# Performance work log

Hardware: AMD Instinct MI355X
Metric: run time of the kernel (lower is better)

Reference implementation:

```python
import jax, jax.numpy as jnp
import numpy as np

EMBED_DIM = 1024
NUM_HEADS = 16
HEAD_DIM = EMBED_DIM // NUM_HEADS
B, S = 2, 2048
NEG = -1e20


def setup_inputs() -> dict:
    key = jax.random.key(0)
    ks = jax.random.split(key, 8)
    scale = 0.02
    return {
        "query": jax.random.normal(ks[0], (B, S, EMBED_DIM), jnp.float32),
        "keys": jax.random.normal(ks[1], (B, S, EMBED_DIM), jnp.float32),
        "values": jax.random.normal(ks[2], (B, S, EMBED_DIM), jnp.float32),
        "mask": jax.random.randint(ks[3], (1, 1, S, S), 0, 2, jnp.int32),
        "Wq": jax.random.normal(ks[4], (EMBED_DIM, EMBED_DIM), jnp.float32) * scale,
        "Wk": jax.random.normal(ks[5], (EMBED_DIM, EMBED_DIM), jnp.float32) * scale,
        "Wv": jax.random.normal(ks[6], (EMBED_DIM, EMBED_DIM), jnp.float32) * scale,
        "Wo": jax.random.normal(ks[7], (EMBED_DIM, EMBED_DIM), jnp.float32) * scale,
        "bo": jnp.zeros((EMBED_DIM,), jnp.float32),
    }


def reference(query, keys, values, mask, Wq, Wk, Wv, Wo, bo):
    N, Lq, _ = query.shape
    Lk = keys.shape[1]
    # torch nn.Linear: y = x @ W.T  (bias=False for Q/K/V)
    Q = (query @ Wq.T).reshape(N, Lq, NUM_HEADS, HEAD_DIM)
    K = (keys @ Wk.T).reshape(N, Lk, NUM_HEADS, HEAD_DIM)
    V = (values @ Wv.T).reshape(N, Lk, NUM_HEADS, HEAD_DIM)
    # NOTE: source scales by sqrt(embed_dim), not sqrt(head_dim) — kept faithful.
    energy = jnp.einsum("nqhd,nkhd->nhqk", Q, K) / jnp.sqrt(
        jnp.asarray(EMBED_DIM, Q.dtype)
    )
    energy = jnp.where(mask == 0, jnp.asarray(NEG, energy.dtype), energy)
    attention = jax.nn.softmax(energy, axis=3)
    out = jnp.einsum("nhqk,nkhd->nqhd", attention, V).reshape(N, Lq, EMBED_DIM)
    return out @ Wo.T + bo
```

## Files before the change

### kernel.cpp

```cpp
#include <hip/hip_runtime.h>
#include <stdint.h>

typedef __bf16 bf16;
typedef __bf16 bf16x4 __attribute__((ext_vector_type(4)));
typedef __bf16 bf16x8 __attribute__((ext_vector_type(8)));
typedef float f32x4 __attribute__((ext_vector_type(4)));
typedef float f32x16 __attribute__((ext_vector_type(16)));
typedef unsigned int uintx2 __attribute__((ext_vector_type(2)));
typedef unsigned int uintx4 __attribute__((ext_vector_type(4)));

#define MFMA16(a, b, c) __builtin_amdgcn_mfma_f32_16x16x32_bf16((a), (b), (c), 0, 0, 0)
#define MFMA32(a, b, c) __builtin_amdgcn_mfma_f32_32x32x16_bf16((a), (b), (c), 0, 0, 0)

__device__ __forceinline__ void gload16(const bf16* g, bf16* l) {
    __builtin_amdgcn_global_load_lds(
        (const __attribute__((address_space(1))) void*)g,
        (__attribute__((address_space(3))) void*)l, 16, 0, 0);
}

__device__ __forceinline__ float fast_exp2(float x) {
#if __has_builtin(__builtin_amdgcn_exp2f)
    return __builtin_amdgcn_exp2f(x);
#else
    return exp2f(x);
#endif
}

__global__ __launch_bounds__(256) void cvt_kernel(
    const float* __restrict__ q, const float* __restrict__ k, const float* __restrict__ v,
    const float* __restrict__ wq, const float* __restrict__ wk,
    const float* __restrict__ wv, const float* __restrict__ wo,
    const int* __restrict__ mask,
    bf16* __restrict__ qb, bf16* __restrict__ kb, bf16* __restrict__ vb,
    bf16* __restrict__ wqb, bf16* __restrict__ wkb, bf16* __restrict__ wvb,
    bf16* __restrict__ wob, unsigned long long* __restrict__ maskb)
{
    int z = blockIdx.z;
    if (z == 7) {
        int t16 = blockIdx.x * 256 + threadIdx.x;
        if (t16 >= 262144) return;
        const int4* mp = (const int4*)mask + (size_t)t16 * 4;
        unsigned bits = 0;
#pragma unroll
        for (int c = 0; c < 4; ++c) {
            int4 a = mp[c];
            bits |= (unsigned)(a.x != 0) << (c * 4 + 0);
            bits |= (unsigned)(a.y != 0) << (c * 4 + 1);
            bits |= (unsigned)(a.z != 0) << (c * 4 + 2);
            bits |= (unsigned)(a.w != 0) << (c * 4 + 3);
        }
        unsigned long long u = (unsigned long long)bits << (16 * (threadIdx.x & 3));
        u |= __shfl_xor(u, 1, 64);
        u |= __shfl_xor(u, 2, 64);
        if ((threadIdx.x & 3) == 0) maskb[t16 >> 2] = u;
        return;
    }
    const float* src; bf16* dst; int n;
    switch (z) {
        case 0:  src = q;  dst = qb;  n = 4194304; break;
        case 1:  src = k;  dst = kb;  n = 4194304; break;
        case 2:  src = v;  dst = vb;  n = 4194304; break;
        case 3:  src = wq; dst = wqb; n = 1048576; break;
        case 4:  src = wk; dst = wkb; n = 1048576; break;
        case 5:  src = wv; dst = wvb; n = 1048576; break;
        default: src = wo; dst = wob; n = 1048576; break;
    }
    int i = (blockIdx.x * 256 + threadIdx.x) * 8;
    if (i >= n) return;
    float4 f0 = *(const float4*)(src + i);
    float4 f1 = *(const float4*)(src + i + 4);
    bf16x8 o;
    o[0] = (bf16)f0.x; o[1] = (bf16)f0.y; o[2] = (bf16)f0.z; o[3] = (bf16)f0.w;
    o[4] = (bf16)f1.x; o[5] = (bf16)f1.y; o[6] = (bf16)f1.z; o[7] = (bf16)f1.w;
    *(bf16x8*)(dst + i) = o;
}

__global__ __launch_bounds__(256) void gemm_qkv_kernel(
    const bf16* __restrict__ A0, const bf16* __restrict__ A1, const bf16* __restrict__ A2,
    const bf16* __restrict__ B0, const bf16* __restrict__ B1, const bf16* __restrict__ B2,
    bf16* __restrict__ C0, bf16* __restrict__ C1, bf16* __restrict__ Vt)
{
    constexpr int BUFSZ = 8192;
    __shared__ bf16 smem[3 * BUFSZ];

    const int f = blockIdx.x + 8 * blockIdx.y + 256 * blockIdx.z;
    const int xcd = f & 7, sidx = f >> 3;
    const int z  = sidx >> 5;
    const int m0 = (xcd * 4 + (sidx & 3)) * 128;
    const int n0 = ((sidx >> 2) & 7) * 128;

    const bf16* A = (z == 0) ? A0 : (z == 1) ? A1 : A2;
    const bf16* B = (z == 0) ? B0 : (z == 1) ? B1 : B2;

    const int tid  = threadIdx.x;
    const int lane = tid & 63;
    const int wave = tid >> 6;
    const int quad = lane >> 4;
    const int l16  = lane & 15;
    const int wm = (wave >> 1) * 64;
    const int wn = (wave & 1) * 64;

    const int lrow = lane >> 2;
    const int lcol = (lane & 3) * 8;

    f32x4 acc[4][4] = {};

    const bf16* Ag = A + (size_t)(m0 + lrow) * 1024 + lcol;
    const bf16* Bg = B + (size_t)(n0 + lrow) * 1024 + lcol;

    bf16* buf0 = smem;
    bf16* buf1 = smem + BUFSZ;
    bf16* buf2 = smem + 2 * BUFSZ;

    auto stage = [&](bf16* base, int k0) {
#pragma unroll
        for (int j = 0; j < 2; ++j)
            gload16(Ag + (size_t)(wave * 32 + j * 16) * 1024 + k0,
                    base + (wave * 32 + j * 16) * 32);
        bf16* Btb = base + 4096;
#pragma unroll
        for (int j = 0; j < 2; ++j)
            gload16(Bg + (size_t)(wave * 32 + j * 16) * 1024 + k0,
                    Btb + (wave * 32 + j * 16) * 32);
    };

    auto step = [&](bf16* cb, bf16* sb, int k0) {
        if (k0 == 992) {
            asm volatile("s_waitcnt vmcnt(0)" ::: "memory");
        } else {
            asm volatile("s_waitcnt vmcnt(4)" ::: "memory");
        }
        __builtin_amdgcn_s_barrier();
        __builtin_amdgcn_sched_barrier(0);
        if (k0 + 64 < 1024) stage(sb, k0 + 64);

        const bf16* Btb = cb + 4096;
        bf16x8 af[4], bg[4];
#pragma unroll
        for (int i = 0; i < 4; ++i)
            af[i] = *(const bf16x8*)(cb + (wm + i * 16 + l16) * 32 + quad * 8);
#pragma unroll
        for (int j = 0; j < 4; ++j)
            bg[j] = *(const bf16x8*)(Btb + (wn + j * 16 + l16) * 32 + quad * 8);
#pragma unroll
        for (int i = 0; i < 4; ++i)
#pragma unroll
            for (int j = 0; j < 4; ++j)
                acc[i][j] = MFMA16(af[i], bg[j], acc[i][j]);
    };

    stage(buf0, 0);
    stage(buf1, 32);
    for (int k0 = 0; k0 < 960; k0 += 96) {
        step(buf0, buf2, k0);
        step(buf1, buf0, k0 + 32);
        step(buf2, buf1, k0 + 64);
    }
    step(buf0, buf2, 960);
    step(buf1, buf0, 992);

    if (z == 2) {
        __syncthreads();
        const int qsw = ((quad & 1) << 1) | (quad >> 1);
#pragma unroll
        for (int i = 0; i < 4; ++i)
#pragma unroll
            for (int j = 0; j < 4; ++j) {
                int e  = wn + j * 16 + l16;
                int sp = wm + i * 16 + qsw * 4;
                bf16x4 v4;
#pragma unroll
                for (int r = 0; r < 4; ++r) v4[r] = (bf16)acc[i][j][r];
                *(bf16x4*)(smem + e * 136 + sp) = v4;
            }
        __syncthreads();
        const int bq = m0 >> 11;
        const int srow = m0 & 2047;
#pragma unroll
        for (int c = 0; c < 2; ++c) {
            int idx = c * 256 + tid;
            int e = idx >> 2, sc = (idx & 3) * 32;
            bf16* dst = Vt + (size_t)(bq * 1024 + n0 + e) * 2048 + srow + sc;
#pragma unroll
            for (int kk = 0; kk < 4; ++kk)
                *(bf16x8*)(dst + kk * 8) =
                    *(const bf16x8*)(smem + e * 136 + sc + kk * 8);
        }
        return;
    }
    bf16* C = (z == 0) ? C0 : C1;
    const float cs = (z == 0) ? 0.0450842200277800f : 1.0f;
#pragma unroll
    for (int i = 0; i < 4; ++i)
#pragma unroll
        for (int j = 0; j < 4; ++j) {
            int row = m0 + wm + i * 16 + quad * 4;
            int col = n0 + wn + j * 16 + l16;
#pragma unroll
            for (int r = 0; r < 4; ++r)
                C[(row + r) * 1024 + col] = (bf16)(acc[i][j][r] * cs);
        }
}

__global__ __launch_bounds__(512) void gemm_out_kernel(
    const bf16* __restrict__ Ab, const bf16* __restrict__ Bb,
    const float* __restrict__ bias, float* __restrict__ outf)
{
    constexpr int BUFSZ = 4096 + 2048;
    __shared__ bf16 smem[2 * 3 * BUFSZ];

    const int f = blockIdx.x + 8 * blockIdx.y;
    const int xcd = f & 7, sidx = f >> 3;
    const int m0 = (xcd * 4 + (sidx & 3)) * 128;
    const int n0 = (sidx >> 2) * 64;

    const int tid  = threadIdx.x;
    const int lane = tid & 63;
    const int wave = tid >> 6;
    const int half = wave >> 2;
    const int w4   = wave & 3;
    const int quad = lane >> 4;
    const int l16  = lane & 15;
    const int wm = (w4 >> 1) * 64;
    const int wn = (w4 & 1) * 32;

    const int lrow = lane >> 2;
    const int lcol = (lane & 3) * 8;
    const int kbase = half * 512;

    f32x4 acc[4][2] = {};

    const bf16* Ag = Ab + (size_t)(m0 + lrow) * 1024 + lcol + kbase;
    const bf16* Bg = Bb + (size_t)(n0 + lrow) * 1024 + lcol + kbase;

    bf16* hb   = smem + half * 3 * BUFSZ;
    bf16* buf0 = hb;
    bf16* buf1 = hb + BUFSZ;
    bf16* buf2 = hb + 2 * BUFSZ;

    auto stage = [&](bf16* base, int k0) {
#pragma unroll
        for (int j = 0; j < 2; ++j)
            gload16(Ag + (size_t)(w4 * 32 + j * 16) * 1024 + k0,
                    base + (w4 * 32 + j * 16) * 32);
        gload16(Bg + (size_t)(w4 * 16) * 1024 + k0, base + 4096 + (w4 * 16) * 32);
    };

    auto step = [&](bf16* cb, bf16* sb, int k0) {
        if (k0 == 480) {
            asm volatile("s_waitcnt vmcnt(0)" ::: "memory");
        } else {
            asm volatile("s_waitcnt vmcnt(3)" ::: "memory");
        }
        __builtin_amdgcn_s_barrier();
        __builtin_amdgcn_sched_barrier(0);
        if (k0 + 64 < 512) stage(sb, k0 + 64);

        const bf16* Btb = cb + 4096;
        bf16x8 af[4], bg[2];
#pragma unroll
        for (int i = 0; i < 4; ++i)
            af[i] = *(const bf16x8*)(cb + (wm + i * 16 + l16) * 32 + quad * 8);
#pragma unroll
        for (int j = 0; j < 2; ++j)
            bg[j] = *(const bf16x8*)(Btb + (wn + j * 16 + l16) * 32 + quad * 8);
#pragma unroll
        for (int i = 0; i < 4; ++i)
#pragma unroll
            for (int j = 0; j < 2; ++j)
                acc[i][j] = MFMA16(af[i], bg[j], acc[i][j]);
    };

    stage(buf0, 0);
    stage(buf1, 32);
    for (int k0 = 0; k0 < 480; k0 += 96) {
        step(buf0, buf2, k0);
        step(buf1, buf0, k0 + 32);
        step(buf2, buf1, k0 + 64);
    }
    step(buf0, buf1, 480);

    __syncthreads();
    float* ex = (float*)smem + (w4 * 64 + lane) * 4;
    if (half == 1) {
#pragma unroll
        for (int i = 0; i < 4; ++i) {
            *(f32x4*)(ex + (i + 0) * 1024) = acc[i][0];
            *(f32x4*)(ex + (i + 4) * 1024) = acc[i][1];
        }
    }
    __syncthreads();
    if (half == 0) {
#pragma unroll
        for (int i = 0; i < 4; ++i) {
            f32x4 t0 = *(const f32x4*)(ex + (i + 0) * 1024);
            f32x4 t1 = *(const f32x4*)(ex + (i + 4) * 1024);
#pragma unroll
            for (int j = 0; j < 4; ++j) {
                acc[i][0][j] += t0[j];
                acc[i][1][j] += t1[j];
            }
        }
#pragma unroll
        for (int j = 0; j < 2; ++j) {
            int col = n0 + wn + j * 16 + l16;
            float bj = bias[col];
#pragma unroll
            for (int i = 0; i < 4; ++i) {
                int row = m0 + wm + i * 16 + quad * 4;
#pragma unroll
                for (int r = 0; r < 4; ++r)
                    outf[(row + r) * 1024 + col] = acc[i][j][r] + bj;
            }
        }
    }
}

__global__ __launch_bounds__(512, 4) void flash_kernel(
    const bf16* __restrict__ Q, const bf16* __restrict__ K, const bf16* __restrict__ Vt,
    const unsigned long long* __restrict__ maskb, bf16* __restrict__ O)
{
    __shared__ char smem[65536];

    const int tid  = threadIdx.x;
    const int lane = tid & 63;
    const int wave = tid >> 6;
    const int half = wave >> 2;
    const int w4   = wave & 3;
    const int l32  = lane & 31;
    const int hl   = lane >> 5;
    const int l7   = lane & 7;

    const int flat = blockIdx.x + 16 * (blockIdx.y + 16 * blockIdx.z);
    const int xcd  = flat & 7;
    const int slot = flat >> 3;
    const int bh   = xcd * 4 + (slot >> 4);
    const int h  = bh & 15;
    const int b  = bh >> 4;
    const int q0 = (slot & 15) * 128;
    const int qt = q0 + w4 * 32;

    bf16* hbase = (bf16*)smem + half * 16384;
    bf16* K0 = hbase;
    bf16* K1 = hbase + 4096;
    bf16* V0 = hbase + 8192;
    bf16* V1 = hbase + 12288;

    const bf16* Qb = Q + (size_t)(b * 2048 + qt + l32) * 1024 + h * 64 + hl * 8;
    bf16x8 qf[4];
#pragma unroll
    for (int ks = 0; ks < 4; ++ks) qf[ks] = *(const bf16x8*)(Qb + ks * 16);

    bf16x8 ones;
#pragma unroll
    for (int j = 0; j < 8; ++j) ones[j] = (bf16)1.0f;

    f32x16 acc[2] = {};
    f32x16 lacc = {};

    const int dmarow = lane >> 3;
    const int dmacol = (l7 ^ dmarow) * 8;
    const bf16* Kg = K + (size_t)(b * 2048 + w4 * 16 + dmarow) * 1024 + h * 64 + dmacol;
    const bf16* Vg = Vt + (size_t)((b * 16 + h) * 64 + w4 * 16 + dmarow) * 2048 + dmacol;
    const unsigned long long* Mg = maskb + (size_t)(qt + l32) * 32 + half * 16;
    const int kbase = half * 1024;

    auto stage = [&](bf16* Kd, bf16* Vd, int ktAbs) {
        gload16(Kg + (size_t)ktAbs * 1024,       Kd + (w4 * 16) * 64);
        gload16(Kg + (size_t)(ktAbs + 8) * 1024, Kd + (w4 * 16 + 8) * 64);
        gload16(Vg + ktAbs,                      Vd + (w4 * 16) * 64);
        gload16(Vg + ktAbs + 8 * 2048,           Vd + (w4 * 16 + 8) * 64);
    };

    unsigned long long mw = Mg[0];
    stage(K0, V0, kbase);

    auto body = [&](const bf16* Kc, const bf16* Vc, bf16* Kn, bf16* Vn, int it) {
        __syncthreads();
        unsigned long long mw_next = 0;
        if (it + 1 < 16) {
            stage(Kn, Vn, kbase + (it + 1) * 64);
            mw_next = Mg[it + 1];
        }

        bf16x8 pa[4];
#pragma unroll
        for (int t = 0; t < 2; ++t) {
            f32x16 s = {};
            __builtin_amdgcn_s_setprio(1);
#pragma unroll
            for (int ks = 0; ks < 4; ++ks) {
                bf16x8 ka = *(const bf16x8*)(Kc + (t * 32 + l32) * 64 +
                                             (((ks * 2 + hl) ^ l7) * 8));
                s = MFMA32(ka, qf[ks], s);
            }
            __builtin_amdgcn_s_setprio(0);
            unsigned mwt = (unsigned)(mw >> (t * 32 + 4 * hl));
            unsigned W[4][2];
#pragma unroll
            for (int g = 0; g < 4; ++g) {
                bf16x4 pv;
#pragma unroll
                for (int r = 0; r < 4; ++r) {
                    float ev = fast_exp2(s[g * 4 + r]);
                    unsigned msk = (unsigned)((int)(mwt << (31 - (8 * g + r))) >> 31);
                    unsigned evu = __builtin_bit_cast(unsigned, ev) & msk;
                    pv[r] = (bf16)__builtin_bit_cast(float, evu);
                }
                uintx2 u = __builtin_bit_cast(uintx2, pv);
                W[g][0] = u[0];
                W[g][1] = u[1];
            }
#pragma unroll
            for (int kh = 0; kh < 2; ++kh) {
                uintx4 aw = { W[2 * kh][0], W[2 * kh][1],
                              W[2 * kh + 1][0], W[2 * kh + 1][1] };
                pa[t * 2 + kh] = __builtin_bit_cast(bf16x8, aw);
            }
        }

        __builtin_amdgcn_s_setprio(1);
#pragma unroll
        for (int dt = 0; dt < 2; ++dt)
#pragma unroll
            for (int ks = 0; ks < 4; ++ks) {
                bf16x8 vb = *(const bf16x8*)(Vc + (dt * 32 + l32) * 64 +
                                             (((ks * 2 + hl) ^ l7) * 8));
                acc[dt] = MFMA32(pa[ks], vb, acc[dt]);
            }
#pragma unroll
        for (int ks = 0; ks < 4; ++ks)
            lacc = MFMA32(pa[ks], ones, lacc);
        __builtin_amdgcn_s_setprio(0);

        mw = mw_next;
    };

    for (int it = 0; it < 16; it += 2) {
        body(K0, V0, K1, V1, it);
        body(K1, V1, K0, V0, it + 1);
    }

    __syncthreads();
    float* cb = (float*)smem;
    float* ex = cb + (w4 * 64 + lane) * 4;
    if (half == 1) {
#pragma unroll
        for (int i = 0; i < 4; ++i) {
            f32x4 t0, t1, t2;
#pragma unroll
            for (int j = 0; j < 4; ++j) {
                t0[j] = acc[0][i * 4 + j];
                t1[j] = acc[1][i * 4 + j];
                t2[j] = lacc[i * 4 + j];
            }
            *(f32x4*)(ex + (i + 0) * 1024) = t0;
            *(f32x4*)(ex + (i + 4) * 1024) = t1;
            *(f32x4*)(ex + (i + 8) * 1024) = t2;
        }
    }
    __syncthreads();
    if (half == 0) {
#pragma unroll
        for (int i = 0; i < 4; ++i) {
            f32x4 t0 = *(const f32x4*)(ex + (i + 0) * 1024);
            f32x4 t1 = *(const f32x4*)(ex + (i + 4) * 1024);
            f32x4 t2 = *(const f32x4*)(ex + (i + 8) * 1024);
#pragma unroll
            for (int j = 0; j < 4; ++j) {
                acc[0][i * 4 + j] += t0[j];
                acc[1][i * 4 + j] += t1[j];
                lacc[i * 4 + j]   += t2[j];
            }
        }

        const size_t obase = (size_t)(b * 2048 + qt) * 1024 + h * 64;
#pragma unroll
        for (int g = 0; g < 4; ++g)
#pragma unroll
            for (int r = 0; r < 4; ++r) {
                int qr = 4 * hl + 8 * g + r;
                float inv = 1.0f / lacc[g * 4 + r];
                O[obase + (size_t)qr * 1024 + l32]      = (bf16)(acc[0][g * 4 + r] * inv);
                O[obase + (size_t)qr * 1024 + 32 + l32] = (bf16)(acc[1][g * 4 + r] * inv);
            }
    }
}

extern "C" void kernel_launch(void* const* d_in, const int* in_sizes, int n_in,
                              void* d_out, int out_size, void* d_ws, size_t ws_size,
                              hipStream_t stream)
{
    const float* q  = (const float*)d_in[0];
    const float* k  = (const float*)d_in[1];
    const float* v  = (const float*)d_in[2];
    const int* mask = (const int*)d_in[3];
    const float* wq = (const float*)d_in[4];
    const float* wk = (const float*)d_in[5];
    const float* wv = (const float*)d_in[6];
    const float* wo = (const float*)d_in[7];
    const float* bo = (const float*)d_in[8];
    float* out = (float*)d_out;

    char* p = (char*)d_ws;
    auto alloc = [&](size_t bytes) {
        char* r = p;
        p += (bytes + 255) & ~(size_t)255;
        return r;
    };
    const size_t SB = (size_t)4096 * 1024 * 2;
    const size_t WB = (size_t)1024 * 1024 * 2;
    bf16* qb  = (bf16*)alloc(SB);
    bf16* kb  = (bf16*)alloc(SB);
    bf16* vb  = (bf16*)alloc(SB);
    bf16* wqb = (bf16*)alloc(WB);
    bf16* wkb = (bf16*)alloc(WB);
    bf16* wvb = (bf16*)alloc(WB);
    bf16* wob = (bf16*)alloc(WB);
    bf16* Qp  = (bf16*)alloc(SB);
    bf16* Kp  = (bf16*)alloc(SB);
    bf16* Vtp = (bf16*)alloc(SB);
    bf16* Ob  = (bf16*)alloc(SB);
    unsigned long long* maskb = (unsigned long long*)alloc(2048 * 32 * 8);

    cvt_kernel<<<dim3(2048, 1, 8), 256, 0, stream>>>(
        q, k, v, wq, wk, wv, wo, mask, qb, kb, vb, wqb, wkb, wvb, wob, maskb);

    gemm_qkv_kernel<<<dim3(8, 32, 3), 256, 0, stream>>>(
        qb, kb, vb, wqb, wkb, wvb, Qp, Kp, Vtp);

    flash_kernel<<<dim3(16, 16, 2), 512, 0, stream>>>(Qp, Kp, Vtp, maskb, Ob);

    gemm_out_kernel<<<dim3(8, 64), 512, 0, stream>>>(Ob, wob, bo, out);
}
```

Measured before the change: 226.5 us.

## Single-buffer V tile and cut flash kernel LDS to raise occupancy

The V tile goes from double-buffered to a single LDS buffer, shrinking shared memory from 64KB to 48KB, and launch bounds rise to 6 blocks/CU hint. V for the current step is now loaded at the start of each iteration alongside the next K tile, with explicit vmcnt waits and an extra barrier before the PV MFMAs. The goal is more resident waves to hide latency, at the cost of exposing V load latency within each iteration and adding a barrier per step. The mask word is also loaded synchronously each iteration instead of prefetched.

```diff
diff --git a/kernel.cpp b/kernel.cpp
--- a/kernel.cpp
+++ b/kernel.cpp
@@ -316,11 +316,11 @@
     }
 }
 
-__global__ __launch_bounds__(512, 4) void flash_kernel(
+__global__ __launch_bounds__(512, 6) void flash_kernel(
     const bf16* __restrict__ Q, const bf16* __restrict__ K, const bf16* __restrict__ Vt,
     const unsigned long long* __restrict__ maskb, bf16* __restrict__ O)
 {
-    __shared__ char smem[65536];
+    __shared__ char smem[49152];
 
     const int tid  = threadIdx.x;
     const int lane = tid & 63;
@@ -340,11 +340,10 @@
     const int q0 = (slot & 15) * 128;
     const int qt = q0 + w4 * 32;
 
-    bf16* hbase = (bf16*)smem + half * 16384;
+    bf16* hbase = (bf16*)smem + half * 12288;
     bf16* K0 = hbase;
     bf16* K1 = hbase + 4096;
-    bf16* V0 = hbase + 8192;
-    bf16* V1 = hbase + 12288;
+    bf16* Vb = hbase + 8192;
 
     const bf16* Qb = Q + (size_t)(b * 2048 + qt + l32) * 1024 + h * 64 + hl * 8;
     bf16x8 qf[4];
@@ -365,23 +364,26 @@
     const unsigned long long* Mg = maskb + (size_t)(qt + l32) * 32 + half * 16;
     const int kbase = half * 1024;
 
-    auto stage = [&](bf16* Kd, bf16* Vd, int ktAbs) {
+    auto stageK = [&](bf16* Kd, int ktAbs) {
         gload16(Kg + (size_t)ktAbs * 1024,       Kd + (w4 * 16) * 64);
         gload16(Kg + (size_t)(ktAbs + 8) * 1024, Kd + (w4 * 16 + 8) * 64);
-        gload16(Vg + ktAbs,                      Vd + (w4 * 16) * 64);
-        gload16(Vg + ktAbs + 8 * 2048,           Vd + (w4 * 16 + 8) * 64);
-    };
-
-    unsigned long long mw = Mg[0];
-    stage(K0, V0, kbase);
-
-    auto body = [&](const bf16* Kc, const bf16* Vc, bf16* Kn, bf16* Vn, int it) {
-        __syncthreads();
-        unsigned long long mw_next = 0;
-        if (it + 1 < 16) {
-            stage(Kn, Vn, kbase + (it + 1) * 64);
-            mw_next = Mg[it + 1];
-        }
+    };
+    auto stageV = [&](int ktAbs) {
+        gload16(Vg + ktAbs,            Vb + (w4 * 16) * 64);
+        gload16(Vg + ktAbs + 8 * 2048, Vb + (w4 * 16 + 8) * 64);
+    };
+
+    stageK(K0, kbase);
+
+    auto body = [&](const bf16* Kc, bf16* Kn, int it) {
+        asm volatile("s_waitcnt vmcnt(0)" ::: "memory");
+        __builtin_amdgcn_s_barrier();
+        __builtin_amdgcn_sched_barrier(0);
+        unsigned long long mw = Mg[it];
+        __builtin_amdgcn_sched_barrier(0);
+        stageV(kbase + it * 64);
+        if (it + 1 < 16) stageK(Kn, kbase + (it + 1) * 64);
+        __builtin_amdgcn_sched_barrier(0);
 
         bf16x8 pa[4];
 #pragma unroll
@@ -395,6 +397,10 @@
                 s = MFMA32(ka, qf[ks], s);
             }
             __builtin_amdgcn_s_setprio(0);
+            if (t == 0) {
+                if (it == 15) asm volatile("s_waitcnt vmcnt(2)" ::: "memory");
+                else          asm volatile("s_waitcnt vmcnt(4)" ::: "memory");
+            }
             unsigned mwt = (unsigned)(mw >> (t * 32 + 4 * hl));
             unsigned W[4][2];
 #pragma unroll
@@ -419,12 +425,17 @@
             }
         }
 
+        if (it == 15) asm volatile("s_waitcnt vmcnt(0)" ::: "memory");
+        else          asm volatile("s_waitcnt vmcnt(2)" ::: "memory");
+        __builtin_amdgcn_s_barrier();
+        __builtin_amdgcn_sched_barrier(0);
+
         __builtin_amdgcn_s_setprio(1);
 #pragma unroll
         for (int dt = 0; dt < 2; ++dt)
 #pragma unroll
             for (int ks = 0; ks < 4; ++ks) {
-                bf16x8 vb = *(const bf16x8*)(Vc + (dt * 32 + l32) * 64 +
+                bf16x8 vb = *(const bf16x8*)(Vb + (dt * 32 + l32) * 64 +
                                              (((ks * 2 + hl) ^ l7) * 8));
                 acc[dt] = MFMA32(pa[ks], vb, acc[dt]);
             }
@@ -432,13 +443,11 @@
         for (int ks = 0; ks < 4; ++ks)
             lacc = MFMA32(pa[ks], ones, lacc);
         __builtin_amdgcn_s_setprio(0);
-
-        mw = mw_next;
     };
 
     for (int it = 0; it < 16; it += 2) {
-        body(K0, V0, K1, V1, it);
-        body(K1, V1, K0, V0, it + 1);
+        body(K0, K1, it);
+        body(K1, K0, it + 1);
     }
 
     __syncthreads();
```

New measurement: 439.1 us. 93.9% more time.
